# Optimization experiments

Hardware: AMD Instinct MI355X
Metric: run time of the kernel (lower is better)

Reference implementation:

```python
import jax, jax.numpy as jnp
import numpy as np

HEADS = 4
ATTN_MODE = 'strided'
LOCAL_ATTN_CTX = 32
BLOCKSIZE = 32


def strided_transpose(x, n_ctx, local_attn_ctx):
    # [n, t, e] -> [n, bT_ctx, local, e] -> [n, local, bT_ctx, e] -> [n, t, e]
    bT_ctx = n_ctx // local_attn_ctx
    n, t, e = x.shape
    x = x.reshape(n, bT_ctx, local_attn_ctx, e)
    x = jnp.transpose(x, (0, 2, 1, 3))
    return x.reshape(n, t, e)


def setup_inputs() -> dict:
    key = jax.random.key(0)
    kq, kk, kv = jax.random.split(key, 3)
    shape = (2, 4096, 1024)
    return {
        'q': jax.random.normal(kq, shape, dtype=jnp.float32),
        'k': jax.random.normal(kk, shape, dtype=jnp.float32),
        'v': jax.random.normal(kv, shape, dtype=jnp.float32),
    }


def reference(q, k, v):
    n_ctx = q.shape[1]
    if ATTN_MODE == 'strided':
        bT_ctx = n_ctx // LOCAL_ATTN_CTX
        assert bT_ctx % BLOCKSIZE == 0
        q = strided_transpose(q, n_ctx, LOCAL_ATTN_CTX)
        k = strided_transpose(k, n_ctx, LOCAL_ATTN_CTX)
        v = strided_transpose(v, n_ctx, LOCAL_ATTN_CTX)
    n_state = q.shape[-1] // HEADS
    scale = 1.0 / np.sqrt(n_state)
    w = jnp.einsum('nte,nse->nts', q, k)            # [n, t, t] full scores
    w = jax.nn.softmax(w * scale, axis=-1)
    a = jnp.einsum('nts,nse->nte', w, v)
    if ATTN_MODE == 'strided':
        n, t, e = a.shape
        bT_ctx = n_ctx // LOCAL_ATTN_CTX
        a = a.reshape(n, LOCAL_ATTN_CTX, bT_ctx, e)
        a = jnp.transpose(a, (0, 2, 1, 3))
        a = a.reshape(n, t, e)
    return a
```

## Files before the change

kernel.cpp:

```cpp
#include <hip/hip_runtime.h>

using short8  = __attribute__((ext_vector_type(8))) short;
using ushort8 = __attribute__((ext_vector_type(8))) unsigned short;
using f32x4   = __attribute__((ext_vector_type(4))) float;

#define T 4096
#define E 1024
#define NB 2
#define BM 128
#define BN 128
#define BK 32
#define TILE_ELEMS (BM * BK)

__device__ __forceinline__ unsigned short f2bf(float f) {
    unsigned int u = __builtin_bit_cast(unsigned int, f);
    u = (u + 0x7FFFu + ((u >> 16) & 1u)) >> 16;
    return (unsigned short)u;
}

__device__ __forceinline__ void gld16(const unsigned short* g, unsigned short* l) {
    __builtin_amdgcn_global_load_lds(
        (__attribute__((address_space(1))) void*)g,
        (__attribute__((address_space(3))) void*)l, 16, 0, 0);
}

__device__ __forceinline__ void do_cvt(const float* __restrict__ src,
                                       unsigned short* __restrict__ dst, int blk) {
    size_t i = ((size_t)blk * 256 + threadIdx.x) * 8;
    float4 f0 = *(const float4*)(src + i);
    float4 f1 = *(const float4*)(src + i + 4);
    ushort8 u;
    u[0]=f2bf(f0.x); u[1]=f2bf(f0.y); u[2]=f2bf(f0.z); u[3]=f2bf(f0.w);
    u[4]=f2bf(f1.x); u[5]=f2bf(f1.y); u[6]=f2bf(f1.z); u[7]=f2bf(f1.w);
    *(ushort8*)(dst + i) = u;
}

__device__ __forceinline__ void do_vt(const float* __restrict__ v,
                                      unsigned short* __restrict__ vt, int id,
                                      float (*tile)[65]) {
    int b   = id / (64 * 16);
    int rem = id % (64 * 16);
    int t0  = (rem / 16) * 64;
    int e0  = (rem % 16) * 64;
    int tid = threadIdx.x;
    int r   = tid >> 2;
    int c0  = (tid & 3) * 16;
    const float* src = v + ((size_t)(b * T + t0 + r)) * E + e0 + c0;
    #pragma unroll
    for (int i = 0; i < 4; i++) {
        float4 f = *(const float4*)(src + i * 4);
        tile[r][c0 + i*4 + 0] = f.x;
        tile[r][c0 + i*4 + 1] = f.y;
        tile[r][c0 + i*4 + 2] = f.z;
        tile[r][c0 + i*4 + 3] = f.w;
    }
    __syncthreads();
    int er = tid >> 2;
    #pragma unroll
    for (int ch = 0; ch < 2; ch++) {
        int tl = (tid & 3) * 16 + ch * 8;
        ushort8 u;
        #pragma unroll
        for (int j = 0; j < 8; j++) u[j] = f2bf(tile[tl + j][er]);
        *(ushort8*)(vt + ((size_t)(b * E + e0 + er)) * T + t0 + tl) = u;
    }
}

__global__ __launch_bounds__(256) void prep(const float* __restrict__ q,
                                            const float* __restrict__ k,
                                            const float* __restrict__ v,
                                            unsigned short* __restrict__ qb,
                                            unsigned short* __restrict__ kb,
                                            unsigned short* __restrict__ vt,
                                            float* __restrict__ lsum) {
    __shared__ float tile[64][65];
    int bid = blockIdx.x;
    if (bid < 4096)        do_cvt(q, qb, bid);
    else if (bid < 8192)   do_cvt(k, kb, bid - 4096);
    else if (bid < 10240)  do_vt(v, vt, bid - 8192, tile);
    else                   lsum[(bid - 10240) * 256 + threadIdx.x] = 0.0f;
}

__global__ __launch_bounds__(256) void prologue(const float* __restrict__ q,
                                                const float* __restrict__ k,
                                                unsigned short* __restrict__ qb,
                                                unsigned short* __restrict__ kb,
                                                float* __restrict__ lsum) {
    int bid = blockIdx.x;
    if (bid < 4096)      do_cvt(q, qb, bid);
    else if (bid < 8192) do_cvt(k, kb, bid - 4096);
    else                 lsum[(bid - 8192) * 256 + threadIdx.x] = 0.0f;
}
__global__ __launch_bounds__(256) void v_transpose(const float* __restrict__ v,
                                                   unsigned short* __restrict__ vt) {
    __shared__ float tile[64][65];
    do_vt(v, vt, blockIdx.x, tile);
}

template <int KITERS, int NBUF>
__device__ __forceinline__ void gemm_core(const unsigned short* Abase, int apitch,
                                          const unsigned short* Bbase, int bpitch,
                                          unsigned short* ldsA, unsigned short* ldsB,
                                          int tid, f32x4 (&acc)[4][4]) {
    constexpr int D = NBUF - 1;
    const int lane = tid & 63, wave = tid >> 6;
    const int l15 = lane & 15, kq = lane >> 4;
    const int wm = (wave & 1) * 64, wn = (wave >> 1) * 64;

    const unsigned short* ga[2];
    const unsigned short* gb[2];
    int lo[2];
    #pragma unroll
    for (int i = 0; i < 2; i++) {
        int p = i * 256 + tid;
        int r = p >> 2;
        int kqw = (p & 3) ^ ((p >> 3) & 3);
        ga[i] = Abase + (size_t)r * apitch + kqw * 8;
        gb[i] = Bbase + (size_t)r * bpitch + kqw * 8;
        lo[i] = (i * 256 + wave * 64) * 8;
    }
    int aoff[4], boff[4];
    #pragma unroll
    for (int mi = 0; mi < 4; mi++) {
        int r = wm + mi * 16 + l15;
        aoff[mi] = (r * 4 + (kq ^ ((r >> 1) & 3))) * 8;
        int rn = wn + mi * 16 + l15;
        boff[mi] = (rn * 4 + (kq ^ ((rn >> 1) & 3))) * 8;
    }

    #pragma unroll
    for (int i = 0; i < D; i++) {
        gld16(ga[0] + i * BK, ldsA + i * TILE_ELEMS + lo[0]);
        gld16(ga[1] + i * BK, ldsA + i * TILE_ELEMS + lo[1]);
        gld16(gb[0] + i * BK, ldsB + i * TILE_ELEMS + lo[0]);
        gld16(gb[1] + i * BK, ldsB + i * TILE_ELEMS + lo[1]);
    }

    int cbuf = 0, pbuf = D, pkt = D;
    for (int kt = 0; kt < KITERS; kt++) {
        asm volatile("s_barrier" ::: "memory");
        gld16(ga[0] + pkt * BK, ldsA + pbuf * TILE_ELEMS + lo[0]);
        gld16(ga[1] + pkt * BK, ldsA + pbuf * TILE_ELEMS + lo[1]);
        gld16(gb[0] + pkt * BK, ldsB + pbuf * TILE_ELEMS + lo[0]);
        gld16(gb[1] + pkt * BK, ldsB + pbuf * TILE_ELEMS + lo[1]);
        if constexpr (D == 1) asm volatile("s_waitcnt vmcnt(4)" ::: "memory");
        else                  asm volatile("s_waitcnt vmcnt(8)" ::: "memory");
        asm volatile("s_barrier" ::: "memory");

        const unsigned short* A = ldsA + cbuf * TILE_ELEMS;
        const unsigned short* B = ldsB + cbuf * TILE_ELEMS;
        short8 af[4], bf[4];
        #pragma unroll
        for (int i = 0; i < 4; i++) {
            af[i] = *(const short8*)(A + aoff[i]);
            bf[i] = *(const short8*)(B + boff[i]);
        }
        #pragma unroll
        for (int mi = 0; mi < 4; mi++)
            #pragma unroll
            for (int ni = 0; ni < 4; ni++)
                acc[mi][ni] = __builtin_amdgcn_mfma_f32_16x16x32_bf16(af[mi], bf[ni], acc[mi][ni], 0, 0, 0);

        if (++cbuf == NBUF) cbuf = 0;
        if (++pbuf == NBUF) pbuf = 0;
        if (++pkt == KITERS) pkt = 0;
    }
}

__global__ __launch_bounds__(256, 2) void pass1(const unsigned short* __restrict__ qb,
                                                const unsigned short* __restrict__ kb,
                                                unsigned short* __restrict__ P,
                                                float* __restrict__ lsum) {
    __shared__ unsigned short ldsA[3 * TILE_ELEMS];
    __shared__ unsigned short ldsB[3 * TILE_ELEMS];
    const int bx = blockIdx.x;
    const int x = bx & 7, j = bx >> 3;
    const int gm = x * 8 + (j & 7);
    const int nt = j >> 3;
    const int b = gm >> 5, mt = gm & 31;
    const int tid = threadIdx.x;

    f32x4 acc[4][4];
    #pragma unroll
    for (int i = 0; i < 4; i++)
        #pragma unroll
        for (int jj = 0; jj < 4; jj++) acc[i][jj] = {};

    gemm_core<E / BK, 3>(qb + ((size_t)b * T + mt * BM) * E, E,
                         kb + ((size_t)b * T + nt * BN) * E, E,
                         ldsA, ldsB, tid, acc);

    const int lane = tid & 63, wave = tid >> 6;
    const int wm = (wave & 1) * 64, wn = (wave >> 1) * 64;
    const int quad = lane >> 4, l15 = lane & 15;
    const float sl2 = 0.0625f * 1.44269504089f;
    const int col0 = nt * BN + wn + l15;

    #pragma unroll
    for (int mi = 0; mi < 4; mi++) {
        #pragma unroll
        for (int r = 0; r < 4; r++) {
            int row = mt * BM + wm + mi * 16 + quad * 4 + r;
            size_t base = ((size_t)b * T + row) * T + col0;
            float s = 0.0f;
            #pragma unroll
            for (int ni = 0; ni < 4; ni++) {
                float p = exp2f(acc[mi][ni][r] * sl2 - 12.0f);
                P[base + ni * 16] = f2bf(p);
                s += p;
            }
            s += __shfl_xor(s, 1);
            s += __shfl_xor(s, 2);
            s += __shfl_xor(s, 4);
            s += __shfl_xor(s, 8);
            if (l15 == 0) atomicAdd(lsum + b * T + row, s);
        }
    }
}

__global__ __launch_bounds__(256, 2) void pass2(const unsigned short* __restrict__ P,
                                                const unsigned short* __restrict__ vt,
                                                const float* __restrict__ lsum,
                                                float* __restrict__ out) {
    __shared__ unsigned short ldsA[3 * TILE_ELEMS];
    __shared__ unsigned short ldsB[3 * TILE_ELEMS];
    const int bx = blockIdx.x;
    const int x = bx & 7, j = bx >> 3;
    const int gm = x * 8 + (j & 7);
    const int nt = j >> 3;
    const int b = gm >> 5, mt = gm & 31;
    const int tid = threadIdx.x;

    f32x4 acc[4][4];
    #pragma unroll
    for (int i = 0; i < 4; i++)
        #pragma unroll
        for (int jj = 0; jj < 4; jj++) acc[i][jj] = {};

    gemm_core<T / BK, 3>(P + ((size_t)b * T + mt * BM) * T, T,
                         vt + ((size_t)b * E + nt * BN) * T, T,
                         ldsA, ldsB, tid, acc);

    const int lane = tid & 63, wave = tid >> 6;
    const int wm = (wave & 1) * 64, wn = (wave >> 1) * 64;
    const int quad = lane >> 4, l15 = lane & 15;
    const int col0 = nt * BN + wn + l15;

    #pragma unroll
    for (int mi = 0; mi < 4; mi++) {
        #pragma unroll
        for (int r = 0; r < 4; r++) {
            int row = mt * BM + wm + mi * 16 + quad * 4 + r;
            float rl = 1.0f / lsum[b * T + row];
            size_t base = ((size_t)b * T + row) * E + col0;
            #pragma unroll
            for (int ni = 0; ni < 4; ni++)
                out[base + ni * 16] = acc[mi][ni][r] * rl;
        }
    }
}

extern "C" void kernel_launch(void* const* d_in, const int* in_sizes, int n_in,
                              void* d_out, int out_size, void* d_ws, size_t ws_size,
                              hipStream_t stream) {
    const float* q = (const float*)d_in[0];
    const float* k = (const float*)d_in[1];
    const float* v = (const float*)d_in[2];
    float* out = (float*)d_out;

    const size_t QK = (size_t)NB * T * E;
    const size_t PSZ = (size_t)NB * T * T;
    float* lsum = (float*)d_ws;
    unsigned short* qbw = (unsigned short*)((char*)d_ws + 32768);
    unsigned short* kbw = qbw + QK;
    unsigned short* Pw  = kbw + QK;

    const size_t full_need = 32768 + (3 * QK + PSZ) * sizeof(unsigned short);

    if (ws_size >= full_need) {
        unsigned short* vtw = Pw + PSZ;
        prep<<<10272, 256, 0, stream>>>(q, k, v, qbw, kbw, vtw, lsum);
        pass1<<<NB * 32 * 32, 256, 0, stream>>>(qbw, kbw, Pw, lsum);
        pass2<<<NB * 32 * 8, 256, 0, stream>>>(Pw, vtw, lsum, out);
    } else {
        unsigned short* vtw = qbw;
        prologue<<<8224, 256, 0, stream>>>(q, k, qbw, kbw, lsum);
        pass1<<<NB * 32 * 32, 256, 0, stream>>>(qbw, kbw, Pw, lsum);
        v_transpose<<<NB * 64 * 16, 256, 0, stream>>>(v, vtw);
        pass2<<<NB * 32 * 8, 256, 0, stream>>>(Pw, vtw, lsum, out);
    }
}
```

Measured before the change: 308.1 us.

## Widen pass1 QK^T tile to 256x128 with 512-thread blocks and double buffering

```diff
diff --git a/kernel.cpp b/kernel.cpp
--- a/kernel.cpp
+++ b/kernel.cpp
@@ -11,6 +11,7 @@
 #define BN 128
 #define BK 32
 #define TILE_ELEMS (BM * BK)
+#define TILE_A_W   (256 * BK)
 
 __device__ __forceinline__ unsigned short f2bf(float f) {
     unsigned int u = __builtin_bit_cast(unsigned int, f);
@@ -167,17 +168,87 @@
     }
 }
 
-__global__ __launch_bounds__(256, 2) void pass1(const unsigned short* __restrict__ qb,
+template <int KITERS>
+__device__ __forceinline__ void gemm_core_wide(const unsigned short* Abase, int apitch,
+                                               const unsigned short* Bbase, int bpitch,
+                                               unsigned short* ldsA, unsigned short* ldsB,
+                                               int tid, f32x4 (&acc)[4][4]) {
+    const int lane = tid & 63, wave = tid >> 6;
+    const int l15 = lane & 15, kq = lane >> 4;
+    const int wm = (wave & 3) * 64, wn = (wave >> 2) * 64;
+
+    const unsigned short* ga[2];
+    int lao[2];
+    #pragma unroll
+    for (int i = 0; i < 2; i++) {
+        int p = i * 512 + tid;
+        int r = p >> 2;
+        int kqw = (p & 3) ^ ((p >> 3) & 3);
+        ga[i] = Abase + (size_t)r * apitch + kqw * 8;
+        lao[i] = (i * 512 + wave * 64) * 8;
+    }
+    const unsigned short* gb;
+    int lbo;
+    {
+        int p = tid;
+        int r = p >> 2;
+        int kqw = (p & 3) ^ ((p >> 3) & 3);
+        gb = Bbase + (size_t)r * bpitch + kqw * 8;
+        lbo = (wave * 64) * 8;
+    }
+    int aoff[4], boff[4];
+    #pragma unroll
+    for (int mi = 0; mi < 4; mi++) {
+        int r = wm + mi * 16 + l15;
+        aoff[mi] = (r * 4 + (kq ^ ((r >> 1) & 3))) * 8;
+        int rn = wn + mi * 16 + l15;
+        boff[mi] = (rn * 4 + (kq ^ ((rn >> 1) & 3))) * 8;
+    }
+
+    gld16(ga[0], ldsA + lao[0]);
+    gld16(ga[1], ldsA + lao[1]);
+    gld16(gb,    ldsB + lbo);
+
+    int cbuf = 0;
+    for (int kt = 0; kt < KITERS; kt++) {
+        int nxt = (kt + 1 < KITERS) ? (kt + 1) : 0;
+        int obuf = cbuf ^ 1;
+        asm volatile("s_barrier" ::: "memory");
+        gld16(ga[0] + nxt * BK, ldsA + obuf * TILE_A_W + lao[0]);
+        gld16(ga[1] + nxt * BK, ldsA + obuf * TILE_A_W + lao[1]);
+        gld16(gb    + nxt * BK, ldsB + obuf * TILE_ELEMS + lbo);
+        asm volatile("s_waitcnt vmcnt(3)" ::: "memory");
+        asm volatile("s_barrier" ::: "memory");
+
+        const unsigned short* A = ldsA + cbuf * TILE_A_W;
+        const unsigned short* B = ldsB + cbuf * TILE_ELEMS;
+        short8 af[4], bf[4];
+        #pragma unroll
+        for (int i = 0; i < 4; i++) {
+            af[i] = *(const short8*)(A + aoff[i]);
+            bf[i] = *(const short8*)(B + boff[i]);
+        }
+        #pragma unroll
+        for (int mi = 0; mi < 4; mi++)
+            #pragma unroll
+            for (int ni = 0; ni < 4; ni++)
+                acc[mi][ni] = __builtin_amdgcn_mfma_f32_16x16x32_bf16(af[mi], bf[ni], acc[mi][ni], 0, 0, 0);
+
+        cbuf = obuf;
+    }
+}
+
+__global__ __launch_bounds__(512, 2) void pass1(const unsigned short* __restrict__ qb,
                                                 const unsigned short* __restrict__ kb,
                                                 unsigned short* __restrict__ P,
                                                 float* __restrict__ lsum) {
-    __shared__ unsigned short ldsA[3 * TILE_ELEMS];
-    __shared__ unsigned short ldsB[3 * TILE_ELEMS];
+    __shared__ unsigned short ldsA[2 * TILE_A_W];
+    __shared__ unsigned short ldsB[2 * TILE_ELEMS];
     const int bx = blockIdx.x;
     const int x = bx & 7, j = bx >> 3;
-    const int gm = x * 8 + (j & 7);
-    const int nt = j >> 3;
-    const int b = gm >> 5, mt = gm & 31;
+    const int gm = x * 4 + (j & 3);
+    const int nt = j >> 2;
+    const int b = gm >> 4, mt = gm & 15;
     const int tid = threadIdx.x;
 
     f32x4 acc[4][4];
@@ -186,12 +257,12 @@
         #pragma unroll
         for (int jj = 0; jj < 4; jj++) acc[i][jj] = {};
 
-    gemm_core<E / BK, 3>(qb + ((size_t)b * T + mt * BM) * E, E,
-                         kb + ((size_t)b * T + nt * BN) * E, E,
-                         ldsA, ldsB, tid, acc);
+    gemm_core_wide<E / BK>(qb + ((size_t)b * T + mt * 256) * E, E,
+                           kb + ((size_t)b * T + nt * BN) * E, E,
+                           ldsA, ldsB, tid, acc);
 
     const int lane = tid & 63, wave = tid >> 6;
-    const int wm = (wave & 1) * 64, wn = (wave >> 1) * 64;
+    const int wm = (wave & 3) * 64, wn = (wave >> 2) * 64;
     const int quad = lane >> 4, l15 = lane & 15;
     const float sl2 = 0.0625f * 1.44269504089f;
     const int col0 = nt * BN + wn + l15;
@@ -200,7 +271,7 @@
     for (int mi = 0; mi < 4; mi++) {
         #pragma unroll
         for (int r = 0; r < 4; r++) {
-            int row = mt * BM + wm + mi * 16 + quad * 4 + r;
+            int row = mt * 256 + wm + mi * 16 + quad * 4 + r;
             size_t base = ((size_t)b * T + row) * T + col0;
             float s = 0.0f;
             #pragma unroll
@@ -280,12 +351,12 @@
     if (ws_size >= full_need) {
         unsigned short* vtw = Pw + PSZ;
         prep<<<10272, 256, 0, stream>>>(q, k, v, qbw, kbw, vtw, lsum);
-        pass1<<<NB * 32 * 32, 256, 0, stream>>>(qbw, kbw, Pw, lsum);
+        pass1<<<1024, 512, 0, stream>>>(qbw, kbw, Pw, lsum);
         pass2<<<NB * 32 * 8, 256, 0, stream>>>(Pw, vtw, lsum, out);
     } else {
         unsigned short* vtw = qbw;
         prologue<<<8224, 256, 0, stream>>>(q, k, qbw, kbw, lsum);
-        pass1<<<NB * 32 * 32, 256, 0, stream>>>(qbw, kbw, Pw, lsum);
+        pass1<<<1024, 512, 0, stream>>>(qbw, kbw, Pw, lsum);
         v_transpose<<<NB * 64 * 16, 256, 0, stream>>>(v, vtw);
         pass2<<<NB * 32 * 8, 256, 0, stream>>>(Pw, vtw, lsum, out);
     }
```

After: 294.5 us. 4.4% less time.
